# Optimization experiments

Measured on AMD Instinct MI355X. Metric: run time of the kernel, lower is better.

Reference implementation:

```python
import jax, jax.numpy as jnp
import numpy as np

ALPHA = 0.2  # LeakyReLU negative slope
NEG_INF = -9e15  # matches torch's -9000000000000000.0 mask value


def setup_inputs() -> dict:
    key = jax.random.key(0)
    k1, k2, k3, k4 = jax.random.split(key, 4)
    B, M, F = 8, 1024, 256
    H, E = 8, F // 8  # attention_heads, out_features
    x = jax.random.normal(k1, (B, M, F), dtype=jnp.float32)
    adj = jax.random.randint(k2, (B, M, M), 0, 2, dtype=jnp.int32)
    weight = jax.random.normal(k3, (H, F, E), dtype=jnp.float32)
    att = jax.random.normal(k4, (H, 2 * E, 1), dtype=jnp.float32)
    return {"x": x, "adj": adj, "weight": weight, "att": att}


def reference(x, adj, weight, att):
    # x: [B, M, F], adj: [B, M, M], weight: [H, F, E], att: [H, 2E, 1]
    B, M, _ = x.shape
    H, _, E = weight.shape
    Wh = jnp.einsum('bmf,hfe->bhme', x, weight)  # [B, H, M, E]
    # Decompose the repeat+concat score: e_ij = a1.Wh_i + a2.Wh_j
    a1 = att[:, :E, 0]   # [H, E]
    a2 = att[:, E:, 0]   # [H, E]
    s1 = jnp.einsum('bhme,he->bhm', Wh, a1)
    s2 = jnp.einsum('bhme,he->bhm', Wh, a2)
    e = s1[:, :, :, None] + s2[:, :, None, :]  # [B, H, M, M]
    e = jnp.where(e > 0, e, ALPHA * e)  # LeakyReLU
    e = jnp.where(adj[:, None, :, :] > 0, e, NEG_INF)
    attn = jax.nn.softmax(e, axis=-1)  # [B, H, M, M]
    h = jnp.einsum('bhmn,bhne->bhme', attn, Wh)  # [B, H, M, E]
    out = h.transpose(0, 2, 1, 3).reshape(B, M, H * E)  # concat heads
    out = jax.nn.elu(out)  # res_pre_act path (dropout is identity in eval)
    return out
```

## Files before the change

### kernel.cpp

```cpp
#include <hip/hip_runtime.h>
#include <stdint.h>

#define ALPHA 0.2f
#define LOG2E 1.44269504089f

typedef __attribute__((ext_vector_type(8))) short s16x8;
typedef __attribute__((ext_vector_type(4))) float f32x4;
typedef __attribute__((ext_vector_type(4))) unsigned u32x4;

__device__ __forceinline__ unsigned short f2bf(float f) {
    union { float f; unsigned u; } c; c.f = f;
    unsigned u = c.u;
    u += 0x7fffu + ((u >> 16) & 1u);
    return (unsigned short)(u >> 16);
}

__global__ void k_prep_w(const float* __restrict__ weight, const float* __restrict__ att,
                         unsigned short* __restrict__ wT, float* __restrict__ wa1,
                         float* __restrict__ wa2) {
    int blk = blockIdx.x, t = threadIdx.x;
    if (blk < 256) {
        int c = blk, h = c >> 5, e = c & 31;
        wT[c * 256 + t] = f2bf(weight[h * 8192 + t * 32 + e]);
    } else {
        int id = blk - 256, h = id >> 1, which = id & 1;
        float s = 0.f;
        for (int e = 0; e < 32; ++e)
            s += weight[h * 8192 + t * 32 + e] * att[h * 64 + which * 32 + e];
        s *= LOG2E;
        (which ? wa2 : wa1)[h * 256 + t] = s;
    }
}

__global__ void __launch_bounds__(512) k_pre(const int* __restrict__ adj,
                                             unsigned* __restrict__ gmask,
                                             const float* __restrict__ x,
                                             unsigned short* __restrict__ x16,
                                             const float* __restrict__ wa1,
                                             const float* __restrict__ wa2,
                                             float* __restrict__ s1,
                                             float* __restrict__ s2) {
    __shared__ unsigned char adjb[16][1024];
    __shared__ float xs[16][260];
    int blk = blockIdx.x;
    int t = threadIdx.x, w = t >> 6, l = t & 63;
    const int* abase = adj + blk * 16384;
#pragma unroll
    for (int it = 0; it < 8; ++it) {
        int f = it * 512 + t;
        int4 v = *(const int4*)(abase + f * 4);
        int row = f >> 8, col = (f & 255) * 4;
        unsigned p1 = __builtin_amdgcn_perm((unsigned)v.y, (unsigned)v.x, 0x00000400u);
        unsigned p2 = __builtin_amdgcn_perm((unsigned)v.w, (unsigned)v.z, 0x00000400u);
        unsigned pk = __builtin_amdgcn_perm(p2, p1, 0x05040100u);
        *(unsigned*)&adjb[row][col ^ ((row & 7) << 4)] = pk;
    }
    const float* xbase = x + blk * 4096;
#pragma unroll
    for (int it = 0; it < 2; ++it) {
        int f = it * 512 + t;
        float4 xv = *(const float4*)(xbase + f * 4);
        int row = f >> 6, col = (f & 63) * 4;
        *(float4*)&xs[row][col] = xv;
        ushort4 hv;
        hv.x = f2bf(xv.x); hv.y = f2bf(xv.y); hv.z = f2bf(xv.z); hv.w = f2bf(xv.w);
        *(ushort4*)&x16[blk * 4096 + f * 4] = hv;
    }
    __syncthreads();
    if (w < 4) {
        for (int k = 0; k < 64; ++k) {
            int task = w * 64 + k;
            int row = task >> 4, ch = task & 15;
            unsigned char byv = adjb[row][(ch * 64 + l) ^ ((row & 7) << 4)];
            unsigned long long mk = __ballot(byv != 0);
            if (l == 0) {
                unsigned* dst = gmask + (blk * 16 + row) * 32 + ch * 2;
                dst[0] = (unsigned)mk;
                dst[1] = (unsigned)(mk >> 32);
            }
        }
    } else {
        int td = (w - 4) * 64 + l;
        int row = td & 15, grp = td >> 4;
        int h = grp >> 1, which = grp & 1;
        const float* wap = (which ? wa2 : wa1) + h * 256;
        float s = 0.f;
#pragma unroll 4
        for (int f = 0; f < 256; f += 4) {
            f32x4 xv = *(const f32x4*)&xs[row][f];
            f32x4 wv = *(const f32x4*)&wap[f];
            s += xv[0] * wv[0] + xv[1] * wv[1] + xv[2] * wv[2] + xv[3] * wv[3];
        }
        int b = blk >> 6, m = (blk & 63) * 16 + row;
        (which ? s2 : s1)[(b * 8 + h) * 1024 + m] = s;
    }
}

__global__ void k_wht(const unsigned short* __restrict__ wT,
                      const unsigned short* __restrict__ x16,
                      unsigned short* __restrict__ WhT) {
    int t = threadIdx.x;
    int W = blockIdx.x * 4 + (t >> 6);
    int l = t & 63;
    int b = W >> 9, r = W & 511;
    int c0 = (r >> 5) * 16, m0 = (r & 31) * 32;
    int lrow = l & 15, lk = l >> 4;
    f32x4 acc[2] = {{0,0,0,0},{0,0,0,0}};
    const unsigned short* ap = wT + (c0 + lrow) * 256 + lk * 8;
    const unsigned short* bp = x16 + (b * 1024 + m0 + lrow) * 256 + lk * 8;
    for (int k0 = 0; k0 < 256; k0 += 32) {
        s16x8 af = *(const s16x8*)(ap + k0);
#pragma unroll
        for (int t4 = 0; t4 < 2; ++t4) {
            s16x8 bf = *(const s16x8*)(bp + t4 * 16 * 256 + k0);
            acc[t4] = __builtin_amdgcn_mfma_f32_16x16x32_bf16(af, bf, acc[t4], 0, 0, 0);
        }
    }
#pragma unroll
    for (int t4 = 0; t4 < 2; ++t4)
#pragma unroll
        for (int j = 0; j < 4; ++j) {
            int c = c0 + lk * 4 + j;
            int m = m0 + t4 * 16 + lrow;
            WhT[(b * 256 + c) * 1024 + m] = f2bf(acc[t4][j]);
        }
}

__global__ void __launch_bounds__(256, 4) k_attn(const unsigned* __restrict__ gmask,
                                                 const float* __restrict__ s1,
                                                 const float* __restrict__ s2,
                                                 const unsigned short* __restrict__ WhT,
                                                 float* __restrict__ out) {
    __shared__ float s2s[2][1024];
    __shared__ unsigned amaskw[16][36];
    __shared__ float s1s[2][16];
    __shared__ float mxsh[2][16][2];
    __shared__ float accsh[2][64][13];
    int bid = blockIdx.x;
    int o = (bid & 7) * 256 + (bid >> 3);
    int b = o >> 8, r = o & 255;
    int m0 = (r >> 2) * 16, hg = (r & 3) * 2;
    int t = threadIdx.x, w = t >> 6, l = t & 63;
    int hd = w & 1, nh = w >> 1;
    for (int i = t; i < 2048; i += 256) s2s[i >> 10][i & 1023] = s2[b * 8192 + hg * 1024 + i];
    for (int i = t; i < 512; i += 256) amaskw[i >> 5][i & 31] = gmask[(b * 1024 + m0) * 32 + i];
    if (t < 32) s1s[t >> 4][t & 15] = s1[b * 8192 + (hg + (t >> 4)) * 1024 + m0 + (t & 15)];
    __syncthreads();
    int m = l & 15, q = l >> 4;
    int h = hg + hd;
    int nbase = nh * 512;
    u32x4 mv0 = *(const u32x4*)&amaskw[m][nh * 16];
    u32x4 mv1 = *(const u32x4*)&amaskw[m][nh * 16 + 4];
    u32x4 mv2 = *(const u32x4*)&amaskw[m][nh * 16 + 8];
    u32x4 mv3 = *(const u32x4*)&amaskw[m][nh * 16 + 12];
    float mxa0 = -3.0e38f, mxa1 = -3.0e38f, mxa2 = -3.0e38f, mxa3 = -3.0e38f;
    float mxa4 = -3.0e38f, mxa5 = -3.0e38f, mxa6 = -3.0e38f, mxa7 = -3.0e38f;
#pragma unroll
    for (int i = 0; i < 16; ++i) {
        unsigned word = (i < 4 ? mv0[i & 3] : i < 8 ? mv1[i & 3] : i < 12 ? mv2[i & 3]
                                                                          : mv3[i & 3]);
        unsigned wm8 = word >> (q * 8);
        int nn = nbase + i * 32 + q * 8;
        f32x4 svA = *(const f32x4*)&s2s[hd][nn];
        f32x4 svB = *(const f32x4*)&s2s[hd][nn + 4];
        mxa0 = fmaxf(mxa0, (wm8 & 1u)   ? svA[0] : -3.0e38f);
        mxa1 = fmaxf(mxa1, (wm8 & 2u)   ? svA[1] : -3.0e38f);
        mxa2 = fmaxf(mxa2, (wm8 & 4u)   ? svA[2] : -3.0e38f);
        mxa3 = fmaxf(mxa3, (wm8 & 8u)   ? svA[3] : -3.0e38f);
        mxa4 = fmaxf(mxa4, (wm8 & 16u)  ? svB[0] : -3.0e38f);
        mxa5 = fmaxf(mxa5, (wm8 & 32u)  ? svB[1] : -3.0e38f);
        mxa6 = fmaxf(mxa6, (wm8 & 64u)  ? svB[2] : -3.0e38f);
        mxa7 = fmaxf(mxa7, (wm8 & 128u) ? svB[3] : -3.0e38f);
    }
    float mxs2 = fmaxf(fmaxf(fmaxf(mxa0, mxa1), fmaxf(mxa2, mxa3)),
                       fmaxf(fmaxf(mxa4, mxa5), fmaxf(mxa6, mxa7)));
    mxs2 = fmaxf(mxs2, __shfl_xor(mxs2, 16));
    mxs2 = fmaxf(mxs2, __shfl_xor(mxs2, 32));
    if (l < 16) mxsh[hd][l][nh] = mxs2;
    __syncthreads();
    float mxf = fmaxf(mxsh[hd][m][0], mxsh[hd][m][1]);
    float s1v = s1s[hd][m];
    float mxr = s1v + mxf;
    float mx = fmaxf(mxr, ALPHA * mxr);
    float c1 = s1v - mx;
    float c2 = fmaf(ALPHA, s1v, -mx);
    f32x4 acc0 = {0,0,0,0}, acc1 = {0,0,0,0}, accs = {0,0,0,0};
    s16x8 ones;
#pragma unroll
    for (int u = 0; u < 8; ++u) ones[u] = (short)0x3F80;
    const unsigned short* bp0 = WhT + (b * 8 + h) * 32768 + m * 1024 + q * 8 + nbase;
    const unsigned short* bp1 = bp0 + 16 * 1024;
#pragma unroll
    for (int i = 0; i < 16; ++i) {
        int n0 = i * 32;
        unsigned word = (i < 4 ? mv0[i & 3] : i < 8 ? mv1[i & 3] : i < 12 ? mv2[i & 3]
                                                                          : mv3[i & 3]);
        unsigned wm8 = word >> (q * 8);
        int nn = nbase + n0 + q * 8;
        f32x4 svA = *(const f32x4*)&s2s[hd][nn];
        f32x4 svB = *(const f32x4*)&s2s[hd][nn + 4];
        float pv[8];
#pragma unroll
        for (int u = 0; u < 8; ++u) {
            float sv = (u < 4 ? svA[u] : svB[u - 4]);
            float arg = fmaxf(sv + c1, fmaf(ALPHA, sv, c2));
            arg = ((wm8 >> u) & 1u) ? arg : -3.0e38f;
            pv[u] = __builtin_amdgcn_exp2f(arg);
        }
        u32x4 aw;
#pragma unroll
        for (int p = 0; p < 4; ++p) {
            union { float f; unsigned u; } lo, hi;
            lo.f = pv[2 * p]; hi.f = pv[2 * p + 1];
            aw[p] = __builtin_amdgcn_perm(hi.u, lo.u, 0x07060302u);
        }
        s16x8 af = __builtin_bit_cast(s16x8, aw);
        s16x8 bf0 = *(const s16x8*)(bp0 + n0);
        s16x8 bf1 = *(const s16x8*)(bp1 + n0);
        acc0 = __builtin_amdgcn_mfma_f32_16x16x32_bf16(af, bf0, acc0, 0, 0, 0);
        acc1 = __builtin_amdgcn_mfma_f32_16x16x32_bf16(af, bf1, acc1, 0, 0, 0);
        accs = __builtin_amdgcn_mfma_f32_16x16x32_bf16(af, ones, accs, 0, 0, 0);
    }
    if (nh == 1) {
#pragma unroll
        for (int j = 0; j < 4; ++j) {
            accsh[hd][l][j]     = acc0[j];
            accsh[hd][l][4 + j] = acc1[j];
            accsh[hd][l][8 + j] = accs[j];
        }
    }
    __syncthreads();
    if (nh == 0) {
#pragma unroll
        for (int j = 0; j < 4; ++j) {
            float a0 = acc0[j] + accsh[hd][l][j];
            float a1 = acc1[j] + accsh[hd][l][4 + j];
            float as = accs[j] + accsh[hd][l][8 + j];
            float inv = 1.f / as;
            float v0 = a0 * inv;
            float v1 = a1 * inv;
            v0 = v0 > 0.f ? v0 : __expf(v0) - 1.f;
            v1 = v1 > 0.f ? v1 : __expf(v1) - 1.f;
            int mrow = q * 4 + j;
            float* op = &out[(b * 1024 + m0 + mrow) * 256 + h * 32];
            op[m] = v0;
            op[16 + m] = v1;
        }
    }
}

extern "C" void kernel_launch(void* const* d_in, const int* in_sizes, int n_in,
                              void* d_out, int out_size, void* d_ws, size_t ws_size,
                              hipStream_t stream) {
    const float* x      = (const float*)d_in[0];
    const int*   adj    = (const int*)d_in[1];
    const float* weight = (const float*)d_in[2];
    const float* att    = (const float*)d_in[3];

    char* ws = (char*)d_ws;
    unsigned short* wT  = (unsigned short*)(ws);
    unsigned short* x16 = (unsigned short*)(ws + 131072);
    unsigned short* WhT = (unsigned short*)(ws + 4325376);
    float* s1  = (float*)(ws + 8519680);
    float* s2  = (float*)(ws + 8781824);
    float* wa1 = (float*)(ws + 9043968);
    float* wa2 = (float*)(ws + 9052160);
    unsigned* gmask = (unsigned*)(ws + 9060352);
    float* out = (float*)d_out;

    k_prep_w<<<272, 256, 0, stream>>>(weight, att, wT, wa1, wa2);
    k_pre<<<512, 512, 0, stream>>>(adj, gmask, x, x16, wa1, wa2, s1, s2);
    k_wht<<<1024, 256, 0, stream>>>(wT, x16, WhT);
    k_attn<<<2048, 256, 0, stream>>>(gmask, s1, s2, WhT, out);
}
```

Measured before the change: 75.42 us.

## Fuse Wh projection into preprocessing kernel and widen attention blocks to four heads

The bf16 x tile is now kept in swizzled shared memory inside k_pre, and each of the 8 warps computes 32 output channels of Wh for that 16-row tile with MFMA. This removes the separate k_wht launch and the x16 round trip through global memory. k_attn now processes four heads per 512-thread block instead of two, which halves the grid and shares the mask load across more heads. The running-max loop is also restructured into four paired accumulators. The costs are more serialized work inside k_pre, a larger shared-memory footprint for k_attn, and fewer blocks in flight.

```diff
diff --git a/kernel.cpp b/kernel.cpp
--- a/kernel.cpp
+++ b/kernel.cpp
@@ -35,15 +35,18 @@
 __global__ void __launch_bounds__(512) k_pre(const int* __restrict__ adj,
                                              unsigned* __restrict__ gmask,
                                              const float* __restrict__ x,
-                                             unsigned short* __restrict__ x16,
+                                             const unsigned short* __restrict__ wT,
                                              const float* __restrict__ wa1,
                                              const float* __restrict__ wa2,
                                              float* __restrict__ s1,
-                                             float* __restrict__ s2) {
+                                             float* __restrict__ s2,
+                                             unsigned short* __restrict__ WhT) {
     __shared__ unsigned char adjb[16][1024];
     __shared__ float xs[16][260];
+    __shared__ unsigned short x16s[16][256];
     int blk = blockIdx.x;
     int t = threadIdx.x, w = t >> 6, l = t & 63;
+    int b = blk >> 6;
     const int* abase = adj + blk * 16384;
 #pragma unroll
     for (int it = 0; it < 8; ++it) {
@@ -64,7 +67,7 @@
         *(float4*)&xs[row][col] = xv;
         ushort4 hv;
         hv.x = f2bf(xv.x); hv.y = f2bf(xv.y); hv.z = f2bf(xv.z); hv.w = f2bf(xv.w);
-        *(ushort4*)&x16[blk * 4096 + f * 4] = hv;
+        *(ushort4*)((char*)&x16s[0][0] + ((row * 512 + col * 2) ^ ((row & 7) << 4))) = hv;
     }
     __syncthreads();
     if (w < 4) {
@@ -91,60 +94,50 @@
             f32x4 wv = *(const f32x4*)&wap[f];
             s += xv[0] * wv[0] + xv[1] * wv[1] + xv[2] * wv[2] + xv[3] * wv[3];
         }
-        int b = blk >> 6, m = (blk & 63) * 16 + row;
+        int m = (blk & 63) * 16 + row;
         (which ? s2 : s1)[(b * 8 + h) * 1024 + m] = s;
     }
-}
-
-__global__ void k_wht(const unsigned short* __restrict__ wT,
-                      const unsigned short* __restrict__ x16,
-                      unsigned short* __restrict__ WhT) {
-    int t = threadIdx.x;
-    int W = blockIdx.x * 4 + (t >> 6);
-    int l = t & 63;
-    int b = W >> 9, r = W & 511;
-    int c0 = (r >> 5) * 16, m0 = (r & 31) * 32;
     int lrow = l & 15, lk = l >> 4;
-    f32x4 acc[2] = {{0,0,0,0},{0,0,0,0}};
-    const unsigned short* ap = wT + (c0 + lrow) * 256 + lk * 8;
-    const unsigned short* bp = x16 + (b * 1024 + m0 + lrow) * 256 + lk * 8;
-    for (int k0 = 0; k0 < 256; k0 += 32) {
-        s16x8 af = *(const s16x8*)(ap + k0);
-#pragma unroll
-        for (int t4 = 0; t4 < 2; ++t4) {
-            s16x8 bf = *(const s16x8*)(bp + t4 * 16 * 256 + k0);
-            acc[t4] = __builtin_amdgcn_mfma_f32_16x16x32_bf16(af, bf, acc[t4], 0, 0, 0);
-        }
-    }
-#pragma unroll
-    for (int t4 = 0; t4 < 2; ++t4)
+#pragma unroll
+    for (int ct = 0; ct < 2; ++ct) {
+        int c0 = (w * 2 + ct) * 16;
+        f32x4 acc = {0, 0, 0, 0};
+        const unsigned short* ap = wT + (c0 + lrow) * 256 + lk * 8;
+#pragma unroll
+        for (int k0 = 0; k0 < 256; k0 += 32) {
+            s16x8 af = *(const s16x8*)(ap + k0);
+            s16x8 bf = *(const s16x8*)((char*)&x16s[0][0] +
+                        ((lrow * 512 + (lk * 8 + k0) * 2) ^ ((lrow & 7) << 4)));
+            acc = __builtin_amdgcn_mfma_f32_16x16x32_bf16(af, bf, acc, 0, 0, 0);
+        }
 #pragma unroll
         for (int j = 0; j < 4; ++j) {
             int c = c0 + lk * 4 + j;
-            int m = m0 + t4 * 16 + lrow;
-            WhT[(b * 256 + c) * 1024 + m] = f2bf(acc[t4][j]);
-        }
-}
-
-__global__ void __launch_bounds__(256, 4) k_attn(const unsigned* __restrict__ gmask,
+            WhT[(b * 256 + c) * 1024 + (blk & 63) * 16 + lrow] = f2bf(acc[j]);
+        }
+    }
+}
+
+__global__ void __launch_bounds__(512, 4) k_attn(const unsigned* __restrict__ gmask,
                                                  const float* __restrict__ s1,
                                                  const float* __restrict__ s2,
                                                  const unsigned short* __restrict__ WhT,
                                                  float* __restrict__ out) {
-    __shared__ float s2s[2][1024];
+    __shared__ float s2s[4][1024];
     __shared__ unsigned amaskw[16][36];
-    __shared__ float s1s[2][16];
-    __shared__ float mxsh[2][16][2];
-    __shared__ float accsh[2][64][13];
+    __shared__ float s1s[4][16];
+    __shared__ float mxsh[4][16][2];
+    __shared__ float accsh[4][64][13];
     int bid = blockIdx.x;
-    int o = (bid & 7) * 256 + (bid >> 3);
-    int b = o >> 8, r = o & 255;
-    int m0 = (r >> 2) * 16, hg = (r & 3) * 2;
+    int o = (bid & 7) * 128 + (bid >> 3);
+    int b = o >> 7, r = o & 127;
+    int mt = r >> 1, m0 = mt * 16, hg = (r & 1) * 4;
     int t = threadIdx.x, w = t >> 6, l = t & 63;
-    int hd = w & 1, nh = w >> 1;
-    for (int i = t; i < 2048; i += 256) s2s[i >> 10][i & 1023] = s2[b * 8192 + hg * 1024 + i];
-    for (int i = t; i < 512; i += 256) amaskw[i >> 5][i & 31] = gmask[(b * 1024 + m0) * 32 + i];
-    if (t < 32) s1s[t >> 4][t & 15] = s1[b * 8192 + (hg + (t >> 4)) * 1024 + m0 + (t & 15)];
+    int hd = w & 3, nh = w >> 2;
+    for (int i = t; i < 4096; i += 512)
+        s2s[i >> 10][i & 1023] = s2[b * 8192 + hg * 1024 + i];
+    amaskw[t >> 5][t & 31] = gmask[(b * 1024 + m0) * 32 + t];
+    if (t < 64) s1s[t >> 4][t & 15] = s1[b * 8192 + (hg + (t >> 4)) * 1024 + m0 + (t & 15)];
     __syncthreads();
     int m = l & 15, q = l >> 4;
     int h = hg + hd;
@@ -153,8 +146,7 @@
     u32x4 mv1 = *(const u32x4*)&amaskw[m][nh * 16 + 4];
     u32x4 mv2 = *(const u32x4*)&amaskw[m][nh * 16 + 8];
     u32x4 mv3 = *(const u32x4*)&amaskw[m][nh * 16 + 12];
-    float mxa0 = -3.0e38f, mxa1 = -3.0e38f, mxa2 = -3.0e38f, mxa3 = -3.0e38f;
-    float mxa4 = -3.0e38f, mxa5 = -3.0e38f, mxa6 = -3.0e38f, mxa7 = -3.0e38f;
+    float mx01 = -3.0e38f, mx23 = -3.0e38f, mx45 = -3.0e38f, mx67 = -3.0e38f;
 #pragma unroll
     for (int i = 0; i < 16; ++i) {
         unsigned word = (i < 4 ? mv0[i & 3] : i < 8 ? mv1[i & 3] : i < 12 ? mv2[i & 3]
@@ -163,17 +155,20 @@
         int nn = nbase + i * 32 + q * 8;
         f32x4 svA = *(const f32x4*)&s2s[hd][nn];
         f32x4 svB = *(const f32x4*)&s2s[hd][nn + 4];
-        mxa0 = fmaxf(mxa0, (wm8 & 1u)   ? svA[0] : -3.0e38f);
-        mxa1 = fmaxf(mxa1, (wm8 & 2u)   ? svA[1] : -3.0e38f);
-        mxa2 = fmaxf(mxa2, (wm8 & 4u)   ? svA[2] : -3.0e38f);
-        mxa3 = fmaxf(mxa3, (wm8 & 8u)   ? svA[3] : -3.0e38f);
-        mxa4 = fmaxf(mxa4, (wm8 & 16u)  ? svB[0] : -3.0e38f);
-        mxa5 = fmaxf(mxa5, (wm8 & 32u)  ? svB[1] : -3.0e38f);
-        mxa6 = fmaxf(mxa6, (wm8 & 64u)  ? svB[2] : -3.0e38f);
-        mxa7 = fmaxf(mxa7, (wm8 & 128u) ? svB[3] : -3.0e38f);
-    }
-    float mxs2 = fmaxf(fmaxf(fmaxf(mxa0, mxa1), fmaxf(mxa2, mxa3)),
-                       fmaxf(fmaxf(mxa4, mxa5), fmaxf(mxa6, mxa7)));
+        float c0 = (wm8 & 1u)   ? svA[0] : -3.0e38f;
+        float c1 = (wm8 & 2u)   ? svA[1] : -3.0e38f;
+        float c2 = (wm8 & 4u)   ? svA[2] : -3.0e38f;
+        float c3 = (wm8 & 8u)   ? svA[3] : -3.0e38f;
+        float c4 = (wm8 & 16u)  ? svB[0] : -3.0e38f;
+        float c5 = (wm8 & 32u)  ? svB[1] : -3.0e38f;
+        float c6 = (wm8 & 64u)  ? svB[2] : -3.0e38f;
+        float c7 = (wm8 & 128u) ? svB[3] : -3.0e38f;
+        mx01 = fmaxf(mx01, fmaxf(c0, c1));
+        mx23 = fmaxf(mx23, fmaxf(c2, c3));
+        mx45 = fmaxf(mx45, fmaxf(c4, c5));
+        mx67 = fmaxf(mx67, fmaxf(c6, c7));
+    }
+    float mxs2 = fmaxf(fmaxf(mx01, mx23), fmaxf(mx45, mx67));
     mxs2 = fmaxf(mxs2, __shfl_xor(mxs2, 16));
     mxs2 = fmaxf(mxs2, __shfl_xor(mxs2, 32));
     if (l < 16) mxsh[hd][l][nh] = mxs2;
@@ -182,8 +177,8 @@
     float s1v = s1s[hd][m];
     float mxr = s1v + mxf;
     float mx = fmaxf(mxr, ALPHA * mxr);
-    float c1 = s1v - mx;
-    float c2 = fmaf(ALPHA, s1v, -mx);
+    float cc1 = s1v - mx;
+    float cc2 = fmaf(ALPHA, s1v, -mx);
     f32x4 acc0 = {0,0,0,0}, acc1 = {0,0,0,0}, accs = {0,0,0,0};
     s16x8 ones;
 #pragma unroll
@@ -203,7 +198,7 @@
 #pragma unroll
         for (int u = 0; u < 8; ++u) {
             float sv = (u < 4 ? svA[u] : svB[u - 4]);
-            float arg = fmaxf(sv + c1, fmaf(ALPHA, sv, c2));
+            float arg = fmaxf(sv + cc1, fmaf(ALPHA, sv, cc2));
             arg = ((wm8 >> u) & 1u) ? arg : -3.0e38f;
             pv[u] = __builtin_amdgcn_exp2f(arg);
         }
@@ -259,17 +254,15 @@
 
     char* ws = (char*)d_ws;
     unsigned short* wT  = (unsigned short*)(ws);
-    unsigned short* x16 = (unsigned short*)(ws + 131072);
-    unsigned short* WhT = (unsigned short*)(ws + 4325376);
-    float* s1  = (float*)(ws + 8519680);
-    float* s2  = (float*)(ws + 8781824);
-    float* wa1 = (float*)(ws + 9043968);
-    float* wa2 = (float*)(ws + 9052160);
-    unsigned* gmask = (unsigned*)(ws + 9060352);
+    unsigned short* WhT = (unsigned short*)(ws + 131072);
+    float* s1  = (float*)(ws + 4325376);
+    float* s2  = (float*)(ws + 4587520);
+    float* wa1 = (float*)(ws + 4849664);
+    float* wa2 = (float*)(ws + 4857856);
+    unsigned* gmask = (unsigned*)(ws + 4866048);
     float* out = (float*)d_out;
 
     k_prep_w<<<272, 256, 0, stream>>>(weight, att, wT, wa1, wa2);
-    k_pre<<<512, 512, 0, stream>>>(adj, gmask, x, x16, wa1, wa2, s1, s2);
-    k_wht<<<1024, 256, 0, stream>>>(wT, x16, WhT);
-    k_attn<<<2048, 256, 0, stream>>>(gmask, s1, s2, WhT, out);
-}
+    k_pre<<<512, 512, 0, stream>>>(adj, gmask, x, wT, wa1, wa2, s1, s2, WhT);
+    k_attn<<<1024, 512, 0, stream>>>(gmask, s1, s2, WhT, out);
+}
```

New measurement: 68.80 us. 8.8% less time.
